# Kernel optimization log

Measured on AMD Instinct MI355X. Metric: run time of the kernel, lower is better.

Reference implementation:

```python
import jax, jax.numpy as jnp
from jax import lax
import numpy as np

D_MODEL = 1024
D_STATE = 16    # N
D_CONV = 4     # K
EXPAND = 2
D_INNER = EXPAND * D_MODEL          # E = 2048
DT_RANK = -(-D_MODEL // 16)         # ceil(D/16) = 64
BATCH, SEQLEN = 2, 1024


def setup_inputs() -> dict:
    key = jax.random.key(0)
    ks = jax.random.split(key, 12)
    s_in = 1.0 / np.sqrt(D_MODEL)
    s_e = 1.0 / np.sqrt(D_INNER)
    s_r = 1.0 / np.sqrt(DT_RANK)
    x = jax.random.normal(ks[0], (BATCH, SEQLEN, D_MODEL), jnp.float32)
    ln_g = jnp.ones((D_MODEL,), jnp.float32)
    ln_b = jnp.zeros((D_MODEL,), jnp.float32)
    W_in = jax.random.normal(ks[1], (D_MODEL, 2 * D_INNER), jnp.float32) * s_in
    conv_w = jax.random.normal(ks[2], (D_INNER, D_CONV), jnp.float32) * (1.0 / np.sqrt(D_CONV))
    conv_b = jnp.zeros((D_INNER,), jnp.float32)
    W_xp = jax.random.normal(ks[3], (D_INNER, DT_RANK + 2 * D_STATE), jnp.float32) * s_e
    W_dt = jax.random.normal(ks[4], (DT_RANK, D_INNER), jnp.float32) * s_r
    # dt bias init so softplus(b_dt) ~ U[1e-3, 1e-1] (official mamba init)
    dt = jnp.exp(jax.random.uniform(ks[5], (D_INNER,)) * (np.log(0.1) - np.log(1e-3)) + np.log(1e-3))
    b_dt = dt + jnp.log(-jnp.expm1(-dt))  # inverse softplus
    A_log = jnp.log(jnp.broadcast_to(jnp.arange(1, D_STATE + 1, dtype=jnp.float32), (D_INNER, D_STATE)))
    D_param = jnp.ones((D_INNER,), jnp.float32)
    W_out = jax.random.normal(ks[6], (D_INNER, D_MODEL), jnp.float32) * s_e
    res_scale = jnp.ones((1,), jnp.float32)
    return dict(x=x, ln_g=ln_g, ln_b=ln_b, W_in=W_in, conv_w=conv_w, conv_b=conv_b,
                W_xp=W_xp, W_dt=W_dt, b_dt=b_dt, A_log=A_log, D_param=D_param,
                W_out=W_out, res_scale=res_scale)


def _mamba_block(x, ln_g, ln_b, W_in, conv_w, conv_b, W_xp, W_dt, b_dt,
                 A_log, D_param, W_out, res_scale):
    B, L, D = x.shape
    E, N, K, R = D_INNER, D_STATE, D_CONV, DT_RANK
    # --- prenorm (LayerNorm, eps=1e-5) ---
    mu = jnp.mean(x, axis=-1, keepdims=True)
    var = jnp.mean(jnp.square(x - mu), axis=-1, keepdims=True)
    xn = (x - mu) * lax.rsqrt(var + 1e-5) * ln_g + ln_b
    # --- in projection, split into ssm-input u and gate z ---
    xz = jnp.einsum('bld,de->ble', xn, W_in)
    u, z = jnp.split(xz, 2, axis=-1)                      # each [B,L,E]
    # --- causal depthwise conv1d over time + SiLU ---
    uc = u.transpose(0, 2, 1)                             # [B,E,L]
    conv = lax.conv_general_dilated(
        uc, conv_w[:, None, :],                           # [E,1,K]
        window_strides=(1,), padding=[(K - 1, 0)],
        feature_group_count=E,
        dimension_numbers=('NCH', 'OIH', 'NCH'))
    u2 = jax.nn.silu(conv + conv_b[None, :, None]).transpose(0, 2, 1)  # [B,L,E]
    # --- input-dependent dt, B, C ---
    x_dbl = jnp.einsum('ble,er->blr', u2, W_xp)           # [B,L,R+2N]
    dt_lo, Bm, Cm = x_dbl[..., :R], x_dbl[..., R:R + N], x_dbl[..., R + N:]
    dt = jax.nn.softplus(jnp.einsum('blr,re->ble', dt_lo, W_dt) + b_dt)  # [B,L,E]
    A = -jnp.exp(A_log)                                   # [E,N]
    # --- selective scan over time ---
    def step(h, inp):
        dt_t, B_t, C_t, u_t = inp                         # [B,E],[B,N],[B,N],[B,E]
        dA = jnp.exp(dt_t[..., None] * A)                 # [B,E,N]
        h = dA * h + (dt_t * u_t)[..., None] * B_t[:, None, :]
        y_t = jnp.einsum('ben,bn->be', h, C_t)
        return h, y_t
    h0 = jnp.zeros((B, E, N), x.dtype)
    xs = (dt.transpose(1, 0, 2), Bm.transpose(1, 0, 2),
          Cm.transpose(1, 0, 2), u2.transpose(1, 0, 2))
    _, ys = lax.scan(step, h0, xs)                        # ys: [L,B,E]
    y = ys.transpose(1, 0, 2) + u2 * D_param              # skip term D*u
    y = y * jax.nn.silu(z)                                # gating
    out = jnp.einsum('ble,ed->bld', y, W_out)
    # dropout is identity in eval mode
    return x + res_scale * out


def reference(x, ln_g, ln_b, W_in, conv_w, conv_b, W_xp, W_dt, b_dt,
              A_log, D_param, W_out, res_scale):
    return _mamba_block(x, ln_g, ln_b, W_in, conv_w, conv_b, W_xp, W_dt, b_dt,
                        A_log, D_param, W_out, res_scale)
```

## Files before the change

### kernel.cpp

```cpp
#include <hip/hip_runtime.h>
#include <hip/hip_bf16.h>

#define D_MODEL 1024
#define D_STATE 16
#define D_CONV  4
#define D_INNER 2048
#define DT_RANK 64
#define BATCH   2
#define SEQLEN  1024
#define NROWS   (BATCH * SEQLEN)
#define XDBL_W  (DT_RANK + 2 * D_STATE)
#define NCHUNK  64
#define LCHUNK  16
#define NCHAN   (BATCH * D_INNER)
#define KSPLIT_XDBL 8

typedef unsigned short ushort_t;
typedef __attribute__((ext_vector_type(8))) short bf16x8;
typedef __attribute__((ext_vector_type(4))) float f32x4;

__device__ __forceinline__ ushort_t f2bf(float f) {
    union { float f; unsigned u; } v; v.f = f;
    unsigned r = v.u + 0x7fffu + ((v.u >> 16) & 1u);
    return (ushort_t)(r >> 16);
}
__device__ __forceinline__ float bf2f(ushort_t h) {
    union { unsigned u; float f; } v; v.u = (unsigned)h << 16; return v.f;
}
__device__ __forceinline__ float fast_sigmoid(float z) {
    return __builtin_amdgcn_rcpf(1.f + __expf(-z));
}

__global__ __launch_bounds__(256)
void layernorm_kernel(const float* __restrict__ x, const float* __restrict__ g,
                      const float* __restrict__ bb, ushort_t* __restrict__ xnbf)
{
    int row = blockIdx.x;
    const float* xr = x + (size_t)row * D_MODEL;
    int tid = threadIdx.x;
    float4 v = reinterpret_cast<const float4*>(xr)[tid];
    float s  = v.x + v.y + v.z + v.w;
    float ss = v.x * v.x + v.y * v.y + v.z * v.z + v.w * v.w;
    #pragma unroll
    for (int off = 32; off; off >>= 1) {
        s  += __shfl_down(s, off);
        ss += __shfl_down(ss, off);
    }
    __shared__ float sbuf[4], ssbuf[4];
    int wid = tid >> 6, lane = tid & 63;
    if (lane == 0) { sbuf[wid] = s; ssbuf[wid] = ss; }
    __syncthreads();
    if (tid == 0) {
        float st = 0.f, sst = 0.f;
        #pragma unroll
        for (int i = 0; i < 4; ++i) { st += sbuf[i]; sst += ssbuf[i]; }
        sbuf[0] = st; ssbuf[0] = sst;
    }
    __syncthreads();
    float mu  = sbuf[0] * (1.f / D_MODEL);
    float var = ssbuf[0] * (1.f / D_MODEL) - mu * mu;
    float inv = rsqrtf(var + 1e-5f);
    float4 gv = reinterpret_cast<const float4*>(g)[tid];
    float4 bv = reinterpret_cast<const float4*>(bb)[tid];
    ushort4 o;
    o.x = f2bf((v.x - mu) * inv * gv.x + bv.x);
    o.y = f2bf((v.y - mu) * inv * gv.y + bv.y);
    o.z = f2bf((v.z - mu) * inv * gv.z + bv.z);
    o.w = f2bf((v.w - mu) * inv * gv.w + bv.w);
    reinterpret_cast<ushort4*>(xnbf + (size_t)row * D_MODEL)[tid] = o;
}

__global__ __launch_bounds__(256)
void transpose_convert_kernel(const float* __restrict__ W, ushort_t* __restrict__ Wt,
                              int R, int C)
{
    __shared__ float t[32][33];
    int c0 = blockIdx.x * 32, r0 = blockIdx.y * 32;
    int tx = threadIdx.x, ty = threadIdx.y;
    #pragma unroll
    for (int i = 0; i < 32; i += 8)
        t[ty + i][tx] = W[(size_t)(r0 + ty + i) * C + c0 + tx];
    __syncthreads();
    #pragma unroll
    for (int i = 0; i < 32; i += 8)
        Wt[(size_t)(c0 + ty + i) * R + r0 + tx] = f2bf(t[tx][ty + i]);
}

__global__ __launch_bounds__(256)
void pad_zero_kernel(ushort_t* __restrict__ dst)
{
    int i = blockIdx.x * 256 + threadIdx.x;
    reinterpret_cast<ushort4*>(dst)[i] = (ushort4){0, 0, 0, 0};
}

__device__ __forceinline__ void stage128x32(const ushort_t* __restrict__ gbase,
                                            size_t ld, ushort_t* ldsb, int tid)
{
    int l = tid & 63;
    int w = tid >> 6;
    int row = w * 16 + (l >> 2);
    int kg  = l & 3;
    char* lb = (char*)ldsb + w * 1024;
    const ushort_t* g0 = gbase + (size_t)row * ld + kg * 8;
    __builtin_amdgcn_global_load_lds(
        (const __attribute__((address_space(1))) unsigned*)g0,
        (__attribute__((address_space(3))) unsigned*)lb, 16, 0, 0);
    const ushort_t* g1 = g0 + (size_t)64 * ld;
    __builtin_amdgcn_global_load_lds(
        (const __attribute__((address_space(1))) unsigned*)g1,
        (__attribute__((address_space(3))) unsigned*)(lb + 4096), 16, 0, 0);
}

__device__ __forceinline__ void stage64x32(const ushort_t* __restrict__ gbase,
                                           size_t ld, ushort_t* ldsb, int tid)
{
    int l = tid & 63;
    int w = tid >> 6;
    int row = w * 16 + (l >> 2);
    int kg  = l & 3;
    char* lb = (char*)ldsb + w * 1024;
    const ushort_t* g0 = gbase + (size_t)row * ld + kg * 8;
    __builtin_amdgcn_global_load_lds(
        (const __attribute__((address_space(1))) unsigned*)g0,
        (__attribute__((address_space(3))) unsigned*)lb, 16, 0, 0);
}

__global__ __launch_bounds__(256)
void gemm_bf16_mfma_bfout(const ushort_t* __restrict__ A, const ushort_t* __restrict__ Bt,
                          ushort_t* __restrict__ C, int M, int N, int K)
{
    __shared__ ushort_t As[128 * 32];
    __shared__ ushort_t Bs[128 * 32];
    int tid = threadIdx.x;
    int l = tid & 63, wid = tid >> 6;
    int wr = wid >> 1, wc = wid & 1;
    int row0 = blockIdx.y * 128, col0 = blockIdx.x * 128;

    f32x4 acc[4][4];
    #pragma unroll
    for (int m = 0; m < 4; ++m)
        #pragma unroll
        for (int n = 0; n < 4; ++n)
            acc[m][n] = (f32x4){0.f, 0.f, 0.f, 0.f};

    const ushort_t* Ab = A  + (size_t)row0 * K;
    const ushort_t* Bb = Bt + (size_t)col0 * K;
    int arow = wr * 64 + (l & 15);
    int brow = wc * 64 + (l & 15);
    int kb   = (l >> 4) * 8;

    for (int k0 = 0; k0 < K; k0 += 32) {
        stage128x32(Ab + k0, K, As, tid);
        stage128x32(Bb + k0, K, Bs, tid);
        __syncthreads();
        bf16x8 af[4], bfr[4];
        #pragma unroll
        for (int m = 0; m < 4; ++m)
            af[m] = *reinterpret_cast<const bf16x8*>(&As[(arow + m * 16) * 32 + kb]);
        #pragma unroll
        for (int n = 0; n < 4; ++n)
            bfr[n] = *reinterpret_cast<const bf16x8*>(&Bs[(brow + n * 16) * 32 + kb]);
        #pragma unroll
        for (int m = 0; m < 4; ++m)
            #pragma unroll
            for (int n = 0; n < 4; ++n)
                acc[m][n] = __builtin_amdgcn_mfma_f32_16x16x32_bf16(
                    af[m], bfr[n], acc[m][n], 0, 0, 0);
        __syncthreads();
    }

    int ro = (l >> 4) * 4, co = l & 15;
    #pragma unroll
    for (int m = 0; m < 4; ++m) {
        #pragma unroll
        for (int n = 0; n < 4; ++n) {
            int c = col0 + wc * 64 + n * 16 + co;
            #pragma unroll
            for (int reg = 0; reg < 4; ++reg) {
                int r = row0 + wr * 64 + m * 16 + ro + reg;
                C[(size_t)r * N + c] = f2bf(acc[m][n][reg]);
            }
        }
    }
}

__global__ __launch_bounds__(256)
void gemm_bf16_dt(const ushort_t* __restrict__ A, const ushort_t* __restrict__ Bt,
                  ushort_t* __restrict__ dtb, const float* __restrict__ bias)
{
    __shared__ ushort_t As[128 * 32];
    __shared__ ushort_t Bs[128 * 32];
    const int K = DT_RANK;
    int tid = threadIdx.x;
    int l = tid & 63, wid = tid >> 6;
    int wr = wid >> 1, wc = wid & 1;
    int row0 = blockIdx.y * 128, col0 = blockIdx.x * 128;

    f32x4 acc[4][4];
    #pragma unroll
    for (int m = 0; m < 4; ++m)
        #pragma unroll
        for (int n = 0; n < 4; ++n)
            acc[m][n] = (f32x4){0.f, 0.f, 0.f, 0.f};

    const ushort_t* Ab = A  + (size_t)row0 * K;
    const ushort_t* Bb = Bt + (size_t)col0 * K;
    int arow = wr * 64 + (l & 15);
    int brow = wc * 64 + (l & 15);
    int kb   = (l >> 4) * 8;

    #pragma unroll
    for (int k0 = 0; k0 < K; k0 += 32) {
        stage128x32(Ab + k0, K, As, tid);
        stage128x32(Bb + k0, K, Bs, tid);
        __syncthreads();
        bf16x8 af[4], bfr[4];
        #pragma unroll
        for (int m = 0; m < 4; ++m)
            af[m] = *reinterpret_cast<const bf16x8*>(&As[(arow + m * 16) * 32 + kb]);
        #pragma unroll
        for (int n = 0; n < 4; ++n)
            bfr[n] = *reinterpret_cast<const bf16x8*>(&Bs[(brow + n * 16) * 32 + kb]);
        #pragma unroll
        for (int m = 0; m < 4; ++m)
            #pragma unroll
            for (int n = 0; n < 4; ++n)
                acc[m][n] = __builtin_amdgcn_mfma_f32_16x16x32_bf16(
                    af[m], bfr[n], acc[m][n], 0, 0, 0);
        __syncthreads();
    }

    int ro = (l >> 4) * 4, co = l & 15;
    #pragma unroll
    for (int m = 0; m < 4; ++m) {
        #pragma unroll
        for (int n = 0; n < 4; ++n) {
            int c = col0 + wc * 64 + n * 16 + co;
            float bdt = bias[c];
            #pragma unroll
            for (int reg = 0; reg < 4; ++reg) {
                int r = row0 + wr * 64 + m * 16 + ro + reg;
                float v = acc[m][n][reg] + bdt;
                v = (v > 20.f) ? v : __logf(1.f + __expf(v));
                dtb[(size_t)r * D_INNER + c] = f2bf(v);
            }
        }
    }
}

__global__ __launch_bounds__(256)
void gemm_xdbl64(const ushort_t* __restrict__ A, const ushort_t* __restrict__ Bt,
                 float* __restrict__ parts)
{
    __shared__ ushort_t As[64 * 32];
    __shared__ ushort_t Bs[128 * 32];
    const int K = D_INNER;
    const int KS = D_INNER / KSPLIT_XDBL;
    int tid = threadIdx.x;
    int l = tid & 63, wid = tid >> 6;
    int wr = wid >> 1, wc = wid & 1;
    int row0 = blockIdx.y * 64;
    int kbeg = blockIdx.z * KS;

    f32x4 acc[2][4];
    #pragma unroll
    for (int m = 0; m < 2; ++m)
        #pragma unroll
        for (int n = 0; n < 4; ++n)
            acc[m][n] = (f32x4){0.f, 0.f, 0.f, 0.f};

    const ushort_t* Ab = A  + (size_t)row0 * K + kbeg;
    const ushort_t* Bb = Bt + kbeg;
    int arow = wr * 32 + (l & 15);
    int brow = wc * 64 + (l & 15);
    int kb   = (l >> 4) * 8;

    #pragma unroll
    for (int k0 = 0; k0 < KS; k0 += 32) {
        stage64x32(Ab + k0, K, As, tid);
        stage128x32(Bb + k0, K, Bs, tid);
        __syncthreads();
        bf16x8 af[2], bfr[4];
        #pragma unroll
        for (int m = 0; m < 2; ++m)
            af[m] = *reinterpret_cast<const bf16x8*>(&As[(arow + m * 16) * 32 + kb]);
        #pragma unroll
        for (int n = 0; n < 4; ++n)
            bfr[n] = *reinterpret_cast<const bf16x8*>(&Bs[(brow + n * 16) * 32 + kb]);
        #pragma unroll
        for (int m = 0; m < 2; ++m)
            #pragma unroll
            for (int n = 0; n < 4; ++n)
                acc[m][n] = __builtin_amdgcn_mfma_f32_16x16x32_bf16(
                    af[m], bfr[n], acc[m][n], 0, 0, 0);
        __syncthreads();
    }

    float* Cp = parts + (size_t)blockIdx.z * NROWS * XDBL_W;
    int ro = (l >> 4) * 4, co = l & 15;
    #pragma unroll
    for (int m = 0; m < 2; ++m) {
        #pragma unroll
        for (int n = 0; n < 4; ++n) {
            int c = wc * 64 + n * 16 + co;
            if (c >= XDBL_W) continue;
            #pragma unroll
            for (int reg = 0; reg < 4; ++reg) {
                int r = row0 + wr * 32 + m * 16 + ro + reg;
                Cp[(size_t)r * XDBL_W + c] = acc[m][n][reg];
            }
        }
    }
}

__global__ __launch_bounds__(256)
void gemm_out64(const ushort_t* __restrict__ A, const ushort_t* __restrict__ Bt,
                const float* __restrict__ x, const float* __restrict__ res_scale,
                float* __restrict__ out)
{
    __shared__ ushort_t As[64 * 32];
    __shared__ ushort_t Bs[64 * 32];
    const int K = D_INNER, N = D_MODEL;
    int tid = threadIdx.x;
    int l = tid & 63, wid = tid >> 6;
    int wr = wid >> 1, wc = wid & 1;
    int row0 = blockIdx.y * 64, col0 = blockIdx.x * 64;

    f32x4 acc[2][2];
    #pragma unroll
    for (int m = 0; m < 2; ++m)
        #pragma unroll
        for (int n = 0; n < 2; ++n)
            acc[m][n] = (f32x4){0.f, 0.f, 0.f, 0.f};

    const ushort_t* Ab = A  + (size_t)row0 * K;
    const ushort_t* Bb = Bt + (size_t)col0 * K;
    int arow = wr * 32 + (l & 15);
    int brow = wc * 32 + (l & 15);
    int kb   = (l >> 4) * 8;

    for (int k0 = 0; k0 < K; k0 += 32) {
        stage64x32(Ab + k0, K, As, tid);
        stage64x32(Bb + k0, K, Bs, tid);
        __syncthreads();
        bf16x8 af[2], bfr[2];
        #pragma unroll
        for (int m = 0; m < 2; ++m)
            af[m] = *reinterpret_cast<const bf16x8*>(&As[(arow + m * 16) * 32 + kb]);
        #pragma unroll
        for (int n = 0; n < 2; ++n)
            bfr[n] = *reinterpret_cast<const bf16x8*>(&Bs[(brow + n * 16) * 32 + kb]);
        #pragma unroll
        for (int m = 0; m < 2; ++m)
            #pragma unroll
            for (int n = 0; n < 2; ++n)
                acc[m][n] = __builtin_amdgcn_mfma_f32_16x16x32_bf16(
                    af[m], bfr[n], acc[m][n], 0, 0, 0);
        __syncthreads();
    }

    float rs = res_scale[0];
    int ro = (l >> 4) * 4, co = l & 15;
    #pragma unroll
    for (int m = 0; m < 2; ++m) {
        #pragma unroll
        for (int n = 0; n < 2; ++n) {
            int c = col0 + wc * 32 + n * 16 + co;
            #pragma unroll
            for (int reg = 0; reg < 4; ++reg) {
                int r = row0 + wr * 32 + m * 16 + ro + reg;
                out[(size_t)r * N + c] = x[(size_t)r * N + c] + rs * acc[m][n][reg];
            }
        }
    }
}

__global__ __launch_bounds__(256)
void reduce_partials_kernel(const float* __restrict__ p, float* __restrict__ out,
                            ushort_t* __restrict__ out64bf, int n)
{
    int i = blockIdx.x * 256 + threadIdx.x;
    if (i >= n) return;
    float s = 0.f;
    #pragma unroll
    for (int k = 0; k < KSPLIT_XDBL; ++k) s += p[(size_t)k * n + i];
    out[i] = s;
    int r = i / XDBL_W, c = i - r * XDBL_W;
    if (c < DT_RANK) out64bf[r * DT_RANK + c] = f2bf(s);
}

__global__ __launch_bounds__(256)
void conv_silu_kernel(const ushort_t* __restrict__ xzbf, const float* __restrict__ cw,
                      const float* __restrict__ cb, ushort_t* __restrict__ u2bf)
{
    int idx = blockIdx.x * 256 + threadIdx.x;
    int e = idx & (D_INNER - 1);
    int l = (idx >> 11) & (SEQLEN - 1);
    int b = idx >> 21;
    const ushort_t* base = xzbf + (size_t)b * SEQLEN * (2 * D_INNER) + e;
    float w0 = cw[e * 4 + 0], w1 = cw[e * 4 + 1];
    float w2 = cw[e * 4 + 2], w3 = cw[e * 4 + 3];
    float acc = cb[e];
    if (l >= 3) acc += bf2f(base[(size_t)(l - 3) * (2 * D_INNER)]) * w0;
    if (l >= 2) acc += bf2f(base[(size_t)(l - 2) * (2 * D_INNER)]) * w1;
    if (l >= 1) acc += bf2f(base[(size_t)(l - 1) * (2 * D_INNER)]) * w2;
    acc += bf2f(base[(size_t)l * (2 * D_INNER)]) * w3;
    float sv = acc * fast_sigmoid(acc);
    u2bf[idx] = f2bf(sv);
}

__global__ __launch_bounds__(256)
void scan_partial_kernel(const ushort_t* __restrict__ dtb, const float* __restrict__ xdbl,
                         const ushort_t* __restrict__ u2bf,
                         const float* __restrict__ A_log,
                         float* __restrict__ hend, float* __restrict__ sumdt_buf)
{
    int idx = blockIdx.x * 256 + threadIdx.x;
    int p = idx & (NCHAN - 1);
    int c = idx >> 12;
    int b = p >> 11, e = p & (D_INNER - 1);

    float An[D_STATE];
    {
        const float4* ar = reinterpret_cast<const float4*>(A_log + (size_t)e * D_STATE);
        #pragma unroll
        for (int q = 0; q < 4; ++q) {
            float4 a4 = ar[q];
            An[q * 4 + 0] = -__expf(a4.x);
            An[q * 4 + 1] = -__expf(a4.y);
            An[q * 4 + 2] = -__expf(a4.z);
            An[q * 4 + 3] = -__expf(a4.w);
        }
    }
    float h[D_STATE];
    #pragma unroll
    for (int n = 0; n < D_STATE; ++n) h[n] = 0.f;
    float sdt = 0.f;

    size_t rowbase = (size_t)b * SEQLEN + c * LCHUNK;
    #pragma unroll
    for (int j = 0; j < LCHUNK; ++j) {
        size_t row = rowbase + j;
        float dt = bf2f(dtb[row * D_INNER + e]);
        float u  = bf2f(u2bf[row * D_INNER + e]);
        float dtu = dt * u;
        sdt += dt;
        const float4* xr = reinterpret_cast<const float4*>(xdbl + row * XDBL_W + DT_RANK);
        float Bv[D_STATE];
        #pragma unroll
        for (int q = 0; q < 4; ++q) {
            float4 b4 = xr[q];
            Bv[q * 4 + 0] = b4.x; Bv[q * 4 + 1] = b4.y;
            Bv[q * 4 + 2] = b4.z; Bv[q * 4 + 3] = b4.w;
        }
        #pragma unroll
        for (int n = 0; n < D_STATE; ++n)
            h[n] = __expf(dt * An[n]) * h[n] + dtu * Bv[n];
    }

    float4* hp = reinterpret_cast<float4*>(hend + ((size_t)p * NCHUNK + c) * D_STATE);
    #pragma unroll
    for (int q = 0; q < 4; ++q)
        hp[q] = (float4){h[q * 4 + 0], h[q * 4 + 1], h[q * 4 + 2], h[q * 4 + 3]};
    sumdt_buf[p * NCHUNK + c] = sdt;
}

__global__ __launch_bounds__(1024)
void scan_combine_kernel(const float* __restrict__ A_log,
                         const float* __restrict__ sumdt_buf,
                         float* __restrict__ hend )
{
    __shared__ float Ps[NCHUNK][D_STATE];
    __shared__ float Hs[NCHUNK][D_STATE];
    int tid = threadIdx.x;
    int c = tid >> 4, n = tid & 15;
    int p = blockIdx.x;
    int e = p & (D_INNER - 1);
    float An = -__expf(A_log[e * D_STATE + n]);
    float P = __expf(An * sumdt_buf[p * NCHUNK + c]);
    float H = hend[(size_t)p * (NCHUNK * D_STATE) + c * D_STATE + n];
    Ps[c][n] = P; Hs[c][n] = H;
    __syncthreads();
    #pragma unroll
    for (int d = 1; d < NCHUNK; d <<= 1) {
        float Pl = 1.f, Hl = 0.f;
        if (c >= d) { Pl = Ps[c - d][n]; Hl = Hs[c - d][n]; }
        __syncthreads();
        H = P * Hl + H;
        P = P * Pl;
        Ps[c][n] = P; Hs[c][n] = H;
        __syncthreads();
    }
    float carry = (c == 0) ? 0.f : Hs[c - 1][n];
    hend[(size_t)p * (NCHUNK * D_STATE) + c * D_STATE + n] = carry;
}

__global__ __launch_bounds__(256)
void scan_final_kernel(const ushort_t* __restrict__ dtb, const float* __restrict__ xdbl,
                       const ushort_t* __restrict__ xzbf, const ushort_t* __restrict__ u2bf,
                       ushort_t* __restrict__ ybf,
                       const float* __restrict__ A_log,
                       const float* __restrict__ D_param,
                       const float* __restrict__ hcarry)
{
    int idx = blockIdx.x * 256 + threadIdx.x;
    int p = idx & (NCHAN - 1);
    int c = idx >> 12;
    int b = p >> 11, e = p & (D_INNER - 1);
    float De = D_param[e];

    float An[D_STATE];
    {
        const float4* ar = reinterpret_cast<const float4*>(A_log + (size_t)e * D_STATE);
        #pragma unroll
        for (int q = 0; q < 4; ++q) {
            float4 a4 = ar[q];
            An[q * 4 + 0] = -__expf(a4.x);
            An[q * 4 + 1] = -__expf(a4.y);
            An[q * 4 + 2] = -__expf(a4.z);
            An[q * 4 + 3] = -__expf(a4.w);
        }
    }
    float h[D_STATE];
    {
        const float4* hp = reinterpret_cast<const float4*>(
            hcarry + ((size_t)p * NCHUNK + c) * D_STATE);
        #pragma unroll
        for (int q = 0; q < 4; ++q) {
            float4 h4 = hp[q];
            h[q * 4 + 0] = h4.x; h[q * 4 + 1] = h4.y;
            h[q * 4 + 2] = h4.z; h[q * 4 + 3] = h4.w;
        }
    }

    size_t rowbase = (size_t)b * SEQLEN + c * LCHUNK;
    #pragma unroll
    for (int j = 0; j < LCHUNK; ++j) {
        size_t row = rowbase + j;
        float dt = bf2f(dtb[row * D_INNER + e]);
        float u  = bf2f(u2bf[row * D_INNER + e]);
        float dtu = dt * u;
        const float4* xr = reinterpret_cast<const float4*>(xdbl + row * XDBL_W + DT_RANK);
        float Bv[D_STATE], Cv[D_STATE];
        #pragma unroll
        for (int q = 0; q < 4; ++q) {
            float4 b4 = xr[q];
            Bv[q * 4 + 0] = b4.x; Bv[q * 4 + 1] = b4.y;
            Bv[q * 4 + 2] = b4.z; Bv[q * 4 + 3] = b4.w;
            float4 c4 = xr[q + 4];
            Cv[q * 4 + 0] = c4.x; Cv[q * 4 + 1] = c4.y;
            Cv[q * 4 + 2] = c4.z; Cv[q * 4 + 3] = c4.w;
        }
        float y = 0.f;
        #pragma unroll
        for (int n = 0; n < D_STATE; ++n) {
            h[n] = __expf(dt * An[n]) * h[n] + dtu * Bv[n];
            y += h[n] * Cv[n];
        }
        float z  = bf2f(xzbf[row * (2 * D_INNER) + D_INNER + e]);
        float sz = z * fast_sigmoid(z);
        ybf[row * D_INNER + e] = f2bf((y + u * De) * sz);
    }
}

extern "C" void kernel_launch(void* const* d_in, const int* in_sizes, int n_in,
                              void* d_out, int out_size, void* d_ws, size_t ws_size,
                              hipStream_t stream)
{
    const float* x       = (const float*)d_in[0];
    const float* ln_g    = (const float*)d_in[1];
    const float* ln_b    = (const float*)d_in[2];
    const float* W_in    = (const float*)d_in[3];
    const float* conv_w  = (const float*)d_in[4];
    const float* conv_b  = (const float*)d_in[5];
    const float* W_xp    = (const float*)d_in[6];
    const float* W_dt    = (const float*)d_in[7];
    const float* b_dt    = (const float*)d_in[8];
    const float* A_log   = (const float*)d_in[9];
    const float* D_param = (const float*)d_in[10];
    const float* W_out   = (const float*)d_in[11];
    const float* res_sc  = (const float*)d_in[12];
    float* out = (float*)d_out;

    char* ws = (char*)d_ws;
    const size_t MB = 1024 * 1024;
    ushort_t* xzbf   = (ushort_t*)(ws);
    ushort_t* u2bf   = (ushort_t*)(ws + 16 * MB);
    ushort_t* dtb16  = (ushort_t*)(ws + 24 * MB);
    float*    xdbl   = (float*)(ws + 32 * MB);
    ushort_t* xdbl64 = (ushort_t*)(ws + 33 * MB);
    float*    hend   = (float*)(ws + 34 * MB);
    float*    sumdt  = (float*)(ws + 50 * MB);
    ushort_t* xnbf   = (ushort_t*)(ws + 51 * MB);
    ushort_t* WtIn   = (ushort_t*)(ws + 55 * MB);
    ushort_t* WtOut  = (ushort_t*)(ws + 63 * MB);
    ushort_t* WtXp   = (ushort_t*)(ws + 67 * MB);
    ushort_t* WtDt   = (ushort_t*)(ws + 67 * MB + 512 * 1024);
    ushort_t* ybf    = (ushort_t*)(ws + 68 * MB);
    float*    partsX = (float*)(ws + 76 * MB);

    {
        dim3 blk(32, 8);
        dim3 g1((2 * D_INNER) / 32, D_MODEL / 32);
        transpose_convert_kernel<<<g1, blk, 0, stream>>>(W_in, WtIn, D_MODEL, 2 * D_INNER);
        dim3 g2(D_MODEL / 32, D_INNER / 32);
        transpose_convert_kernel<<<g2, blk, 0, stream>>>(W_out, WtOut, D_INNER, D_MODEL);
        dim3 g3(XDBL_W / 32, D_INNER / 32);
        transpose_convert_kernel<<<g3, blk, 0, stream>>>(W_xp, WtXp, D_INNER, XDBL_W);
        dim3 g4(D_INNER / 32, DT_RANK / 32);
        transpose_convert_kernel<<<g4, blk, 0, stream>>>(W_dt, WtDt, DT_RANK, D_INNER);
        pad_zero_kernel<<<64, 256, 0, stream>>>(WtXp + (size_t)XDBL_W * D_INNER);
    }

    layernorm_kernel<<<NROWS, 256, 0, stream>>>(x, ln_g, ln_b, xnbf);

    {
        dim3 grid((2 * D_INNER) / 128, NROWS / 128);
        gemm_bf16_mfma_bfout<<<grid, 256, 0, stream>>>(
            xnbf, WtIn, xzbf, NROWS, 2 * D_INNER, D_MODEL);
    }

    conv_silu_kernel<<<(BATCH * SEQLEN * D_INNER) / 256, 256, 0, stream>>>(
        xzbf, conv_w, conv_b, u2bf);

    {
        dim3 grid(1, NROWS / 64, KSPLIT_XDBL);
        gemm_xdbl64<<<grid, 256, 0, stream>>>(u2bf, WtXp, partsX);
        reduce_partials_kernel<<<(NROWS * XDBL_W + 255) / 256, 256, 0, stream>>>(
            partsX, xdbl, xdbl64, NROWS * XDBL_W);
    }

    {
        dim3 grid(D_INNER / 128, NROWS / 128);
        gemm_bf16_dt<<<grid, 256, 0, stream>>>(xdbl64, WtDt, dtb16, b_dt);
    }

    scan_partial_kernel<<<(NCHAN * NCHUNK) / 256, 256, 0, stream>>>(
        dtb16, xdbl, u2bf, A_log, hend, sumdt);
    scan_combine_kernel<<<NCHAN, 1024, 0, stream>>>(A_log, sumdt, hend);
    scan_final_kernel<<<(NCHAN * NCHUNK) / 256, 256, 0, stream>>>(
        dtb16, xdbl, xzbf, u2bf, ybf, A_log, D_param, hend);

    {
        dim3 grid(D_MODEL / 64, NROWS / 64);
        gemm_out64<<<grid, 256, 0, stream>>>(ybf, WtOut, x, res_sc, out);
    }
}
```

Measured before the change: 175.0 us.

## Fuse prologue kernels, swizzle GEMM blocks, deepen out-GEMM K tile, vectorize conv

LayerNorm, the four weight transpose/convert launches and the pad-zero launch are merged into one prologue kernel that dispatches on block index, with the XDBL pad produced by zero-filling out-of-range columns. The in-projection and out-projection GEMMs use a 1D grid with a block-index swizzle for better L2 locality. The out GEMM stages 64-wide K tiles so each barrier covers two MFMA steps, halving the number of sync rounds. The conv+SiLU kernel now processes four channels per thread with vector loads. Together these aim to cut launch overhead, barrier count and memory-transaction count.

```diff
diff --git a/kernel.cpp b/kernel.cpp
--- a/kernel.cpp
+++ b/kernel.cpp
@@ -31,55 +31,26 @@
     return __builtin_amdgcn_rcpf(1.f + __expf(-z));
 }
 
-__global__ __launch_bounds__(256)
-void layernorm_kernel(const float* __restrict__ x, const float* __restrict__ g,
-                      const float* __restrict__ bb, ushort_t* __restrict__ xnbf)
-{
-    int row = blockIdx.x;
-    const float* xr = x + (size_t)row * D_MODEL;
-    int tid = threadIdx.x;
-    float4 v = reinterpret_cast<const float4*>(xr)[tid];
-    float s  = v.x + v.y + v.z + v.w;
-    float ss = v.x * v.x + v.y * v.y + v.z * v.z + v.w * v.w;
-    #pragma unroll
-    for (int off = 32; off; off >>= 1) {
-        s  += __shfl_down(s, off);
-        ss += __shfl_down(ss, off);
-    }
-    __shared__ float sbuf[4], ssbuf[4];
-    int wid = tid >> 6, lane = tid & 63;
-    if (lane == 0) { sbuf[wid] = s; ssbuf[wid] = ss; }
-    __syncthreads();
-    if (tid == 0) {
-        float st = 0.f, sst = 0.f;
-        #pragma unroll
-        for (int i = 0; i < 4; ++i) { st += sbuf[i]; sst += ssbuf[i]; }
-        sbuf[0] = st; ssbuf[0] = sst;
-    }
-    __syncthreads();
-    float mu  = sbuf[0] * (1.f / D_MODEL);
-    float var = ssbuf[0] * (1.f / D_MODEL) - mu * mu;
-    float inv = rsqrtf(var + 1e-5f);
-    float4 gv = reinterpret_cast<const float4*>(g)[tid];
-    float4 bv = reinterpret_cast<const float4*>(bb)[tid];
-    ushort4 o;
-    o.x = f2bf((v.x - mu) * inv * gv.x + bv.x);
-    o.y = f2bf((v.y - mu) * inv * gv.y + bv.y);
-    o.z = f2bf((v.z - mu) * inv * gv.z + bv.z);
-    o.w = f2bf((v.w - mu) * inv * gv.w + bv.w);
-    reinterpret_cast<ushort4*>(xnbf + (size_t)row * D_MODEL)[tid] = o;
-}
-
-__global__ __launch_bounds__(256)
-void transpose_convert_kernel(const float* __restrict__ W, ushort_t* __restrict__ Wt,
-                              int R, int C)
-{
-    __shared__ float t[32][33];
-    int c0 = blockIdx.x * 32, r0 = blockIdx.y * 32;
-    int tx = threadIdx.x, ty = threadIdx.y;
-    #pragma unroll
-    for (int i = 0; i < 32; i += 8)
-        t[ty + i][tx] = W[(size_t)(r0 + ty + i) * C + c0 + tx];
+#define PRO_LN1   2048
+#define PRO_TIN1  6144
+#define PRO_TOUT1 8192
+#define PRO_TXP1  8448
+#define PRO_TOTAL 8576
+
+__device__ __forceinline__ void transpose_job(const float* __restrict__ W,
+                                              ushort_t* __restrict__ Wt,
+                                              int R, int Creal,
+                                              int cx, int ry, int tid,
+                                              float t[32][33])
+{
+    int c0 = cx * 32, r0 = ry * 32;
+    int tx = tid & 31, ty = tid >> 5;
+    int col = c0 + tx;
+    #pragma unroll
+    for (int i = 0; i < 32; i += 8) {
+        float v = (col < Creal) ? W[(size_t)(r0 + ty + i) * Creal + col] : 0.f;
+        t[ty + i][tx] = v;
+    }
     __syncthreads();
     #pragma unroll
     for (int i = 0; i < 32; i += 8)
@@ -87,10 +58,62 @@
 }
 
 __global__ __launch_bounds__(256)
-void pad_zero_kernel(ushort_t* __restrict__ dst)
-{
-    int i = blockIdx.x * 256 + threadIdx.x;
-    reinterpret_cast<ushort4*>(dst)[i] = (ushort4){0, 0, 0, 0};
+void prologue_kernel(const float* __restrict__ x, const float* __restrict__ g,
+                     const float* __restrict__ bb, ushort_t* __restrict__ xnbf,
+                     const float* __restrict__ W_in, ushort_t* __restrict__ WtIn,
+                     const float* __restrict__ W_out, ushort_t* __restrict__ WtOut,
+                     const float* __restrict__ W_xp, ushort_t* __restrict__ WtXp,
+                     const float* __restrict__ W_dt, ushort_t* __restrict__ WtDt)
+{
+    __shared__ float t[32][33];
+    __shared__ float red[8];
+    int bid = blockIdx.x;
+    int tid = threadIdx.x;
+
+    if (bid < PRO_LN1) {
+        const float* xr = x + (size_t)bid * D_MODEL;
+        float4 v = reinterpret_cast<const float4*>(xr)[tid];
+        float s  = v.x + v.y + v.z + v.w;
+        float ss = v.x * v.x + v.y * v.y + v.z * v.z + v.w * v.w;
+        #pragma unroll
+        for (int off = 32; off; off >>= 1) {
+            s  += __shfl_down(s, off);
+            ss += __shfl_down(ss, off);
+        }
+        int wid = tid >> 6, lane = tid & 63;
+        if (lane == 0) { red[wid] = s; red[4 + wid] = ss; }
+        __syncthreads();
+        if (tid == 0) {
+            float st = 0.f, sst = 0.f;
+            #pragma unroll
+            for (int i = 0; i < 4; ++i) { st += red[i]; sst += red[4 + i]; }
+            red[0] = st; red[4] = sst;
+        }
+        __syncthreads();
+        float mu  = red[0] * (1.f / D_MODEL);
+        float var = red[4] * (1.f / D_MODEL) - mu * mu;
+        float inv = rsqrtf(var + 1e-5f);
+        float4 gv = reinterpret_cast<const float4*>(g)[tid];
+        float4 bv = reinterpret_cast<const float4*>(bb)[tid];
+        ushort4 o;
+        o.x = f2bf((v.x - mu) * inv * gv.x + bv.x);
+        o.y = f2bf((v.y - mu) * inv * gv.y + bv.y);
+        o.z = f2bf((v.z - mu) * inv * gv.z + bv.z);
+        o.w = f2bf((v.w - mu) * inv * gv.w + bv.w);
+        reinterpret_cast<ushort4*>(xnbf + (size_t)bid * D_MODEL)[tid] = o;
+    } else if (bid < PRO_TIN1) {
+        int j = bid - PRO_LN1;
+        transpose_job(W_in, WtIn, D_MODEL, 2 * D_INNER, j & 127, j >> 7, tid, t);
+    } else if (bid < PRO_TOUT1) {
+        int j = bid - PRO_TIN1;
+        transpose_job(W_out, WtOut, D_INNER, D_MODEL, j & 31, j >> 5, tid, t);
+    } else if (bid < PRO_TXP1) {
+        int j = bid - PRO_TOUT1;
+        transpose_job(W_xp, WtXp, D_INNER, XDBL_W, j & 3, j >> 2, tid, t);
+    } else {
+        int j = bid - PRO_TXP1;
+        transpose_job(W_dt, WtDt, DT_RANK, D_INNER, j & 63, j >> 6, tid, t);
+    }
 }
 
 __device__ __forceinline__ void stage128x32(const ushort_t* __restrict__ gbase,
@@ -125,16 +148,36 @@
         (__attribute__((address_space(3))) unsigned*)lb, 16, 0, 0);
 }
 
-__global__ __launch_bounds__(256)
-void gemm_bf16_mfma_bfout(const ushort_t* __restrict__ A, const ushort_t* __restrict__ Bt,
-                          ushort_t* __restrict__ C, int M, int N, int K)
+__device__ __forceinline__ void stage64x64(const ushort_t* __restrict__ gbase,
+                                           size_t ld, ushort_t* ldsb, int tid)
+{
+    int l = tid & 63;
+    int w = tid >> 6;
+    #pragma unroll
+    for (int i = 0; i < 2; ++i) {
+        int row = i * 32 + w * 8 + (l >> 3);
+        const ushort_t* src = gbase + (size_t)row * ld + (l & 7) * 8;
+        char* dst = (char*)ldsb + (i * 32 + w * 8) * 128;
+        __builtin_amdgcn_global_load_lds(
+            (const __attribute__((address_space(1))) unsigned*)src,
+            (__attribute__((address_space(3))) unsigned*)dst, 16, 0, 0);
+    }
+}
+
+__global__ __launch_bounds__(256)
+void gemm_xz(const ushort_t* __restrict__ A, const ushort_t* __restrict__ Bt,
+             ushort_t* __restrict__ C)
 {
     __shared__ ushort_t As[128 * 32];
     __shared__ ushort_t Bs[128 * 32];
+    const int K = D_MODEL, N = 2 * D_INNER;
+    int bid = blockIdx.x;
+    int swz = ((bid & 7) << 6) + (bid >> 3);
+    int bx = swz & 31, by = swz >> 5;
     int tid = threadIdx.x;
     int l = tid & 63, wid = tid >> 6;
     int wr = wid >> 1, wc = wid & 1;
-    int row0 = blockIdx.y * 128, col0 = blockIdx.x * 128;
+    int row0 = by * 128, col0 = bx * 128;
 
     f32x4 acc[4][4];
     #pragma unroll
@@ -318,13 +361,16 @@
                 const float* __restrict__ x, const float* __restrict__ res_scale,
                 float* __restrict__ out)
 {
-    __shared__ ushort_t As[64 * 32];
-    __shared__ ushort_t Bs[64 * 32];
+    __shared__ ushort_t As[64 * 64];
+    __shared__ ushort_t Bs[64 * 64];
     const int K = D_INNER, N = D_MODEL;
+    int bid = blockIdx.x;
+    int swz = ((bid & 7) << 6) + (bid >> 3);
+    int bx = swz & 15, by = swz >> 4;
     int tid = threadIdx.x;
     int l = tid & 63, wid = tid >> 6;
     int wr = wid >> 1, wc = wid & 1;
-    int row0 = blockIdx.y * 64, col0 = blockIdx.x * 64;
+    int row0 = by * 64, col0 = bx * 64;
 
     f32x4 acc[2][2];
     #pragma unroll
@@ -339,23 +385,28 @@
     int brow = wc * 32 + (l & 15);
     int kb   = (l >> 4) * 8;
 
-    for (int k0 = 0; k0 < K; k0 += 32) {
-        stage64x32(Ab + k0, K, As, tid);
-        stage64x32(Bb + k0, K, Bs, tid);
-        __syncthreads();
-        bf16x8 af[2], bfr[2];
-        #pragma unroll
-        for (int m = 0; m < 2; ++m)
-            af[m] = *reinterpret_cast<const bf16x8*>(&As[(arow + m * 16) * 32 + kb]);
-        #pragma unroll
-        for (int n = 0; n < 2; ++n)
-            bfr[n] = *reinterpret_cast<const bf16x8*>(&Bs[(brow + n * 16) * 32 + kb]);
-        #pragma unroll
-        for (int m = 0; m < 2; ++m)
+    for (int k0 = 0; k0 < K; k0 += 64) {
+        stage64x64(Ab + k0, K, As, tid);
+        stage64x64(Bb + k0, K, Bs, tid);
+        __syncthreads();
+        #pragma unroll
+        for (int ks = 0; ks < 2; ++ks) {
+            bf16x8 af[2], bfr[2];
+            #pragma unroll
+            for (int m = 0; m < 2; ++m)
+                af[m] = *reinterpret_cast<const bf16x8*>(
+                    &As[(arow + m * 16) * 64 + ks * 32 + kb]);
             #pragma unroll
             for (int n = 0; n < 2; ++n)
-                acc[m][n] = __builtin_amdgcn_mfma_f32_16x16x32_bf16(
-                    af[m], bfr[n], acc[m][n], 0, 0, 0);
+                bfr[n] = *reinterpret_cast<const bf16x8*>(
+                    &Bs[(brow + n * 16) * 64 + ks * 32 + kb]);
+            #pragma unroll
+            for (int m = 0; m < 2; ++m)
+                #pragma unroll
+                for (int n = 0; n < 2; ++n)
+                    acc[m][n] = __builtin_amdgcn_mfma_f32_16x16x32_bf16(
+                        af[m], bfr[n], acc[m][n], 0, 0, 0);
+        }
         __syncthreads();
     }
 
@@ -393,20 +444,34 @@
 void conv_silu_kernel(const ushort_t* __restrict__ xzbf, const float* __restrict__ cw,
                       const float* __restrict__ cb, ushort_t* __restrict__ u2bf)
 {
-    int idx = blockIdx.x * 256 + threadIdx.x;
-    int e = idx & (D_INNER - 1);
-    int l = (idx >> 11) & (SEQLEN - 1);
-    int b = idx >> 21;
-    const ushort_t* base = xzbf + (size_t)b * SEQLEN * (2 * D_INNER) + e;
-    float w0 = cw[e * 4 + 0], w1 = cw[e * 4 + 1];
-    float w2 = cw[e * 4 + 2], w3 = cw[e * 4 + 3];
-    float acc = cb[e];
-    if (l >= 3) acc += bf2f(base[(size_t)(l - 3) * (2 * D_INNER)]) * w0;
-    if (l >= 2) acc += bf2f(base[(size_t)(l - 2) * (2 * D_INNER)]) * w1;
-    if (l >= 1) acc += bf2f(base[(size_t)(l - 1) * (2 * D_INNER)]) * w2;
-    acc += bf2f(base[(size_t)l * (2 * D_INNER)]) * w3;
-    float sv = acc * fast_sigmoid(acc);
-    u2bf[idx] = f2bf(sv);
+    int idx4 = blockIdx.x * 256 + threadIdx.x;
+    int e0 = (idx4 & 511) * 4;
+    int l  = (idx4 >> 9) & (SEQLEN - 1);
+    int b  = idx4 >> 19;
+    size_t row = (size_t)b * SEQLEN + l;
+    const ushort_t* base = xzbf + row * (2 * D_INNER) + e0;
+    ushort4 r0 = {0,0,0,0}, r1 = {0,0,0,0}, r2 = {0,0,0,0}, r3;
+    if (l >= 3) r0 = *reinterpret_cast<const ushort4*>(base - 3 * (size_t)(2 * D_INNER));
+    if (l >= 2) r1 = *reinterpret_cast<const ushort4*>(base - 2 * (size_t)(2 * D_INNER));
+    if (l >= 1) r2 = *reinterpret_cast<const ushort4*>(base - 1 * (size_t)(2 * D_INNER));
+    r3 = *reinterpret_cast<const ushort4*>(base);
+    const float4* cwv = reinterpret_cast<const float4*>(cw + (size_t)e0 * 4);
+    float4 cb4 = *reinterpret_cast<const float4*>(cb + e0);
+    const ushort_t* p0 = (const ushort_t*)&r0;
+    const ushort_t* p1 = (const ushort_t*)&r1;
+    const ushort_t* p2 = (const ushort_t*)&r2;
+    const ushort_t* p3 = (const ushort_t*)&r3;
+    const float* cbp = (const float*)&cb4;
+    ushort4 o;
+    ushort_t* op = (ushort_t*)&o;
+    #pragma unroll
+    for (int j = 0; j < 4; ++j) {
+        float4 w = cwv[j];
+        float a = cbp[j] + bf2f(p0[j]) * w.x + bf2f(p1[j]) * w.y
+                         + bf2f(p2[j]) * w.z + bf2f(p3[j]) * w.w;
+        op[j] = f2bf(a * fast_sigmoid(a));
+    }
+    reinterpret_cast<ushort4*>(u2bf)[idx4] = o;
 }
 
 __global__ __launch_bounds__(256)
@@ -599,28 +664,12 @@
     ushort_t* ybf    = (ushort_t*)(ws + 68 * MB);
     float*    partsX = (float*)(ws + 76 * MB);
 
-    {
-        dim3 blk(32, 8);
-        dim3 g1((2 * D_INNER) / 32, D_MODEL / 32);
-        transpose_convert_kernel<<<g1, blk, 0, stream>>>(W_in, WtIn, D_MODEL, 2 * D_INNER);
-        dim3 g2(D_MODEL / 32, D_INNER / 32);
-        transpose_convert_kernel<<<g2, blk, 0, stream>>>(W_out, WtOut, D_INNER, D_MODEL);
-        dim3 g3(XDBL_W / 32, D_INNER / 32);
-        transpose_convert_kernel<<<g3, blk, 0, stream>>>(W_xp, WtXp, D_INNER, XDBL_W);
-        dim3 g4(D_INNER / 32, DT_RANK / 32);
-        transpose_convert_kernel<<<g4, blk, 0, stream>>>(W_dt, WtDt, DT_RANK, D_INNER);
-        pad_zero_kernel<<<64, 256, 0, stream>>>(WtXp + (size_t)XDBL_W * D_INNER);
-    }
-
-    layernorm_kernel<<<NROWS, 256, 0, stream>>>(x, ln_g, ln_b, xnbf);
-
-    {
-        dim3 grid((2 * D_INNER) / 128, NROWS / 128);
-        gemm_bf16_mfma_bfout<<<grid, 256, 0, stream>>>(
-            xnbf, WtIn, xzbf, NROWS, 2 * D_INNER, D_MODEL);
-    }
-
-    conv_silu_kernel<<<(BATCH * SEQLEN * D_INNER) / 256, 256, 0, stream>>>(
+    prologue_kernel<<<PRO_TOTAL, 256, 0, stream>>>(
+        x, ln_g, ln_b, xnbf, W_in, WtIn, W_out, WtOut, W_xp, WtXp, W_dt, WtDt);
+
+    gemm_xz<<<512, 256, 0, stream>>>(xnbf, WtIn, xzbf);
+
+    conv_silu_kernel<<<(BATCH * SEQLEN * D_INNER) / 1024, 256, 0, stream>>>(
         xzbf, conv_w, conv_b, u2bf);
 
     {
@@ -641,8 +690,5 @@
     scan_final_kernel<<<(NCHAN * NCHUNK) / 256, 256, 0, stream>>>(
         dtb16, xdbl, xzbf, u2bf, ybf, A_log, D_param, hend);
 
-    {
-        dim3 grid(D_MODEL / 64, NROWS / 64);
-        gemm_out64<<<grid, 256, 0, stream>>>(ybf, WtOut, x, res_sc, out);
-    }
-}
+    gemm_out64<<<512, 256, 0, stream>>>(ybf, WtOut, x, res_sc, out);
+}
```

Measured after the change: 163.6 us. -6.5%, faster.
